# Optimization experiments

Hardware: AMD Instinct MI355X
Metric: run time of the kernel (lower is better)

The kernel has to match this reference:

```python
import jax, jax.numpy as jnp
import numpy as np


def _conv1x1(x, W, b):
    # 1x1 conv == per-pixel channel matmul: x [B,C,H,W], W [O,C], b [O]
    return jnp.einsum('bchw,oc->bohw', x, W) + b[None, :, None, None]


def setup_inputs() -> dict:
    key = jax.random.key(0)
    ks = jax.random.split(key, 9)
    B, C, H, W = 16, 512, 32, 32
    s = 1.0 / np.sqrt(C)
    inp = {
        'x': jax.random.normal(ks[0], (B, C, H, W), dtype=jnp.float32),
        'Wq': jax.random.normal(ks[1], (C, C), dtype=jnp.float32) * s,
        'bq': jax.random.normal(ks[2], (C,), dtype=jnp.float32) * 0.01,
        'Wk': jax.random.normal(ks[3], (C, C), dtype=jnp.float32) * s,
        'bk': jax.random.normal(ks[4], (C,), dtype=jnp.float32) * 0.01,
        'Wv': jax.random.normal(ks[5], (C, C), dtype=jnp.float32) * s,
        'bv': jax.random.normal(ks[6], (C,), dtype=jnp.float32) * 0.01,
        'Wo': jax.random.normal(ks[7], (C, C), dtype=jnp.float32) * s,
        'bo': jax.random.normal(ks[8], (C,), dtype=jnp.float32) * 0.01,
    }
    return inp


def reference(x, Wq, bq, Wk, bk, Wv, bv, Wo, bo):
    B, C, H, W = x.shape
    q = _conv1x1(x, Wq, bq)
    k = _conv1x1(x, Wk, bk)
    v = _conv1x1(x, Wv, bv)
    hw = H * W
    qf = q.reshape(B, C, hw)  # [B,C,HW]
    kf = k.reshape(B, C, hw)
    vf = v.reshape(B, C, hw)
    # scores[b,i,j] = sum_c q[b,c,i] * k[b,c,j], scaled by c^-0.5
    scores = jnp.einsum('bci,bcj->bij', qf, kf) * (C ** -0.5)
    attn = jax.nn.softmax(scores, axis=2)  # softmax over keys j
    # out[b,c,i] = sum_j v[b,c,j] * attn[b,i,j]
    out = jnp.einsum('bcj,bij->bci', vf, attn).reshape(B, C, H, W)
    out = _conv1x1(out, Wo, bo)
    return x + out
```

## Files before the change

kernel.cpp:

```cpp
#include <hip/hip_runtime.h>
#include <hip/hip_bf16.h>
#include <math.h>


typedef __bf16 bf16x8 __attribute__((ext_vector_type(8)));
typedef float  f32x4  __attribute__((ext_vector_type(4)));

__device__ __forceinline__ unsigned short f2bf(float f) {
    unsigned u = __float_as_uint(f);
    u += 0x7fff + ((u >> 16) & 1);
    return (unsigned short)(u >> 16);
}

__device__ __forceinline__ float bf2f(unsigned short h) {
    return __uint_as_float(((unsigned)h) << 16);
}

__device__ __forceinline__ void gload_lds16(const void* g, void* l) {
    __builtin_amdgcn_global_load_lds(
        (const __attribute__((address_space(1))) void*)g,
        (__attribute__((address_space(3))) void*)l, 16, 0, 0);
}

template<bool OUT_F32, int BIAS_MODE, int RESID, int EXPM>
__global__ __launch_bounds__(256) void gemm_bt_mfma(
    const unsigned short* __restrict__ A, const unsigned short* __restrict__ B,
    void* __restrict__ Cout, const float* __restrict__ bias,
    const unsigned short* __restrict__ resid, float* __restrict__ lsum,
    int M, int N, int K, int ldA, int ldB,
    long sA, long sB, long sC, long sR,
    int ln_nn, int ln_pb)
{
    __shared__ unsigned short Als[2][128 * 32];
    __shared__ unsigned short Bls[2][128 * 32];

    const int L   = blockIdx.x;
    const int xcd = L & 7;
    const int idx = L >> 3;
    const int bz  = xcd * 2 + (idx >> ln_pb);
    const int w   = idx & ((1 << ln_pb) - 1);
    const int m0  = (w >> ln_nn) << 7;
    const int n0  = (w & ((1 << ln_nn) - 1)) << 7;

    A += bz * sA;
    B += bz * sB;

    const int tid  = threadIdx.x;
    const int lane = tid & 63;
    const int wave = tid >> 6;
    const int wm   = wave >> 1;
    const int wn   = wave & 1;

    const int ar = lane >> 2;
    const int ak = (lane & 3) * 8;

    const unsigned short* agp = A + (long)(m0 + wave * 16 + ar) * ldA + ak;
    const unsigned short* bgp = B + (long)(n0 + wave * 16 + ar) * ldB + ak;
    const long aj = 64L * ldA;
    const long bj = 64L * ldB;
    unsigned short* al0  = Als[0] + wave * 512;
    unsigned short* al0h = Als[0] + (wave + 4) * 512;
    unsigned short* al1  = Als[1] + wave * 512;
    unsigned short* al1h = Als[1] + (wave + 4) * 512;
    unsigned short* bl0  = Bls[0] + wave * 512;
    unsigned short* bl0h = Bls[0] + (wave + 4) * 512;
    unsigned short* bl1  = Bls[1] + wave * 512;
    unsigned short* bl1h = Bls[1] + (wave + 4) * 512;

    const int fr = lane & 15;
    const int fq = lane >> 4;

    f32x4 acc[4][4] = {};

    for (int k0 = 0; k0 < K; k0 += 64) {
        gload_lds16(agp,           al0);
        gload_lds16(agp + aj,      al0h);
        gload_lds16(agp + 32,      al1);
        gload_lds16(agp + 32 + aj, al1h);
        gload_lds16(bgp,           bl0);
        gload_lds16(bgp + bj,      bl0h);
        gload_lds16(bgp + 32,      bl1);
        gload_lds16(bgp + 32 + bj, bl1h);
        agp += 64; bgp += 64;
        __syncthreads();

        #pragma unroll
        for (int p = 0; p < 2; ++p) {
            bf16x8 af[4], bfr[4];
            #pragma unroll
            for (int mt = 0; mt < 4; ++mt)
                af[mt] = *(const bf16x8*)&Als[p][(wm * 64 + mt * 16 + fr) * 32 + fq * 8];
            #pragma unroll
            for (int nt = 0; nt < 4; ++nt)
                bfr[nt] = *(const bf16x8*)&Bls[p][(wn * 64 + nt * 16 + fr) * 32 + fq * 8];

            #pragma unroll
            for (int mt = 0; mt < 4; ++mt)
                #pragma unroll
                for (int nt = 0; nt < 4; ++nt)
                    acc[mt][nt] = __builtin_amdgcn_mfma_f32_16x16x32_bf16(
                        af[mt], bfr[nt], acc[mt][nt], 0, 0, 0);
        }
        __syncthreads();
    }

    float* Cf = (float*)Cout + bz * sC;
    unsigned short* Ch = (unsigned short*)Cout + bz * sC;
    if (RESID) resid += bz * sR;

    if (EXPM == 1) {
        float* lrow = lsum + bz * (long)M;
        #pragma unroll
        for (int mt = 0; mt < 4; ++mt) {
            const int row = m0 + wm * 64 + mt * 16 + fq * 4;
            #pragma unroll
            for (int r = 0; r < 4; ++r) {
                float rs = 0.0f;
                #pragma unroll
                for (int nt = 0; nt < 4; ++nt) {
                    const int col = n0 + wn * 64 + nt * 16 + fr;
                    const float e = __expf(acc[mt][nt][r]);
                    rs += e;
                    Ch[(long)(row + r) * N + col] = f2bf(e);
                }
                rs += __shfl_xor(rs, 1);
                rs += __shfl_xor(rs, 2);
                rs += __shfl_xor(rs, 4);
                rs += __shfl_xor(rs, 8);
                if (fr == 0) atomicAdd(&lrow[row + r], rs);
            }
        }
    } else {
        float linv[4][4];
        if (EXPM == 2) {
            const float* lrow = lsum + bz * (long)M;
            #pragma unroll
            for (int mt = 0; mt < 4; ++mt)
                #pragma unroll
                for (int r = 0; r < 4; ++r)
                    linv[mt][r] = 1.0f / lrow[m0 + wm * 64 + mt * 16 + fq * 4 + r];
        }
        #pragma unroll
        for (int nt = 0; nt < 4; ++nt) {
            const int col = n0 + wn * 64 + nt * 16 + fr;
            const float bn = (BIAS_MODE == 2) ? bias[col] : 0.0f;
            #pragma unroll
            for (int mt = 0; mt < 4; ++mt) {
                const int row = m0 + wm * 64 + mt * 16 + fq * 4;
                #pragma unroll
                for (int r = 0; r < 4; ++r) {
                    float val = acc[mt][nt][r] + bn;
                    if (BIAS_MODE == 1) val += bias[row + r];
                    if (EXPM == 2) val *= linv[mt][r];
                    const long idx = (long)(row + r) * N + col;
                    if (RESID == 2) val += bf2f(resid[idx]);
                    if (OUT_F32) Cf[idx] = val;
                    else         Ch[idx] = f2bf(val);
                }
            }
        }
    }
}

__global__ __launch_bounds__(256) void prep_all(
    const float* __restrict__ x,
    unsigned short* __restrict__ xT, unsigned short* __restrict__ xbf,
    const float* __restrict__ Wq, const float* __restrict__ Wk,
    const float* __restrict__ Wv, const float* __restrict__ Wo,
    const float* __restrict__ bq, const float* __restrict__ bk,
    const float* __restrict__ bv, const float* __restrict__ bo,
    unsigned short* __restrict__ Wqb, unsigned short* __restrict__ Wkb,
    unsigned short* __restrict__ Wvob,
    float* __restrict__ biasqk, float* __restrict__ bvo,
    float* __restrict__ lsum)
{
    const float s = 0.044194173824159216f;
    const int b = blockIdx.x;
    const int t = threadIdx.x;

    if (b < 256) {
        __shared__ float Ao[32][33];
        __shared__ float Bv[32][33];
        const int m0 = (b >> 4) * 32;
        const int n0 = (b & 15) * 32;
        const int tx = t & 31;
        const int ty = t >> 5;
        float acc[4] = {0.f, 0.f, 0.f, 0.f};
        for (int k0 = 0; k0 < 512; k0 += 32) {
            #pragma unroll
            for (int i = 0; i < 4; ++i)
                Ao[ty + 8 * i][tx] = Wo[(long)(m0 + ty + 8 * i) * 512 + k0 + tx];
            #pragma unroll
            for (int i = 0; i < 4; ++i)
                Bv[ty + 8 * i][tx] = Wv[(long)(k0 + ty + 8 * i) * 512 + n0 + tx];
            __syncthreads();
            #pragma unroll
            for (int kk = 0; kk < 32; ++kk) {
                const float bvv = Bv[kk][tx];
                #pragma unroll
                for (int i = 0; i < 4; ++i)
                    acc[i] += Ao[ty * 4 + i][kk] * bvv;
            }
            __syncthreads();
        }
        #pragma unroll
        for (int i = 0; i < 4; ++i)
            Wvob[(long)(m0 + ty * 4 + i) * 512 + n0 + tx] = f2bf(acc[i]);
    } else if (b < 264) {
        const int o = (b - 256) * 64 + (t >> 2);
        const int q = t & 3;
        const float4* wrow = (const float4*)(Wo + (long)o * 512 + q * 128);
        const float4* bvv4 = (const float4*)(bv + q * 128);
        float p = 0.f;
        #pragma unroll
        for (int i = 0; i < 32; ++i) {
            const float4 w = wrow[i];
            const float4 v = bvv4[i];
            p += w.x * v.x + w.y * v.y + w.z * v.z + w.w * v.w;
        }
        __shared__ float red[256];
        red[t] = p;
        __syncthreads();
        if (q == 0) bvo[o] = red[t] + red[t + 1] + red[t + 2] + red[t + 3] + bo[o];
    } else if (b == 264) {
        biasqk[t]       = bq[t] * s;
        biasqk[256 + t] = bq[256 + t] * s;
        biasqk[512 + t] = bk[t];
        biasqk[768 + t] = bk[256 + t];
        #pragma unroll
        for (int i = 0; i < 64; ++i) lsum[i * 256 + t] = 0.0f;
    } else if (b < 777) {
        const bool isq = b < 521;
        const float* src = isq ? Wq : Wk;
        unsigned short* dst = isq ? Wqb : Wkb;
        const float m = isq ? s : 1.0f;
        const int i = (((b - 265) & 255) * 256 + t) * 4;
        const float4 f = *(const float4*)(src + i);
        ushort4 h;
        h.x = f2bf(f.x * m); h.y = f2bf(f.y * m);
        h.z = f2bf(f.z * m); h.w = f2bf(f.w * m);
        *(ushort4*)(dst + i) = h;
    } else {
        __shared__ float tl[32][33];
        const int xb = b - 777;
        const int batch = xb >> 9;
        const int rem = xb & 511;
        const int p0 = (rem & 31) * 32;
        const int c0 = (rem >> 5) * 32;
        const float* xp = x + (long)batch * 524288;
        unsigned short* xTb  = xT  + (long)batch * 524288;
        unsigned short* xbfb = xbf + (long)batch * 524288;
        const int tx = t & 31;
        const int ty = t >> 5;
        #pragma unroll
        for (int i = 0; i < 4; ++i) {
            const float v = xp[(long)(c0 + ty + 8 * i) * 1024 + p0 + tx];
            xbfb[(long)(c0 + ty + 8 * i) * 1024 + p0 + tx] = f2bf(v);
            tl[ty + 8 * i][tx] = v;
        }
        __syncthreads();
        #pragma unroll
        for (int i = 0; i < 4; ++i)
            xTb[(long)(p0 + ty + 8 * i) * 512 + c0 + tx] = f2bf(tl[tx][ty + 8 * i]);
    }
}

extern "C" void kernel_launch(void* const* d_in, const int* in_sizes, int n_in,
                              void* d_out, int out_size, void* d_ws, size_t ws_size,
                              hipStream_t stream)
{
    const float* x  = (const float*)d_in[0];
    const float* Wq = (const float*)d_in[1];
    const float* bq = (const float*)d_in[2];
    const float* Wk = (const float*)d_in[3];
    const float* bk = (const float*)d_in[4];
    const float* Wv = (const float*)d_in[5];
    const float* bv = (const float*)d_in[6];
    const float* Wo = (const float*)d_in[7];
    const float* bo = (const float*)d_in[8];
    float* out = (float*)d_out;

    const int Bn = 16, C = 512, HW = 1024;
    const long CHW = (long)C * HW;
    const long SHW = (long)HW * HW;

    unsigned short* xT   = (unsigned short*)d_ws;
    unsigned short* qkT  = xT + Bn * CHW;
    unsigned short* xbf  = qkT + Bn * SHW;
    unsigned short* expS = xbf + Bn * CHW;
    unsigned short* Wqb  = expS + Bn * SHW;
    unsigned short* Wkb  = Wqb + 262144;
    unsigned short* Wvob = Wkb + 262144;
    float* biasqk = (float*)(Wvob + 262144);
    float* bvo    = biasqk + 1024;
    float* lsum   = bvo + 512;
    unsigned short* UT = xT;

    const dim3 blk(256);

    prep_all<<<dim3(8969), blk, 0, stream>>>(
        x, xT, xbf, Wq, Wk, Wv, Wo, bq, bk, bv, bo,
        Wqb, Wkb, Wvob, biasqk, bvo, lsum);

    gemm_bt_mfma<false, 2, 0, 0><<<dim3(1024), blk, 0, stream>>>(
        xT, Wqb, qkT, biasqk, nullptr, nullptr,
        HW, 2 * C, C, C, C, CHW, 0, SHW, 0, 3, 6);

    gemm_bt_mfma<false, 0, 0, 1><<<dim3(1024), blk, 0, stream>>>(
        qkT, qkT + C, expS, nullptr, nullptr, lsum,
        HW, HW, C, 2 * C, 2 * C, SHW, SHW, SHW, 0, 3, 6);

    gemm_bt_mfma<false, 0, 0, 2><<<dim3(512), blk, 0, stream>>>(
        expS, xbf, UT, nullptr, nullptr, lsum,
        HW, C, HW, HW, HW, SHW, CHW, CHW, 0, 2, 5);

    gemm_bt_mfma<true, 1, 2, 0><<<dim3(512), blk, 0, stream>>>(
        Wvob, UT, out, bvo, xbf, nullptr,
        C, HW, C, C, C, 0, CHW, CHW, CHW, 3, 5);
}
```

Before: 222.9 us.

## Reassociate output projection before attention and merge projection GEMMs into one launch

```diff
diff --git a/kernel.cpp b/kernel.cpp
--- a/kernel.cpp
+++ b/kernel.cpp
@@ -22,29 +22,22 @@
         (__attribute__((address_space(3))) void*)l, 16, 0, 0);
 }
 
-template<bool OUT_F32, int BIAS_MODE, int RESID, int EXPM>
-__global__ __launch_bounds__(256) void gemm_bt_mfma(
-    const unsigned short* __restrict__ A, const unsigned short* __restrict__ B,
-    void* __restrict__ Cout, const float* __restrict__ bias,
-    const unsigned short* __restrict__ resid, float* __restrict__ lsum,
-    int M, int N, int K, int ldA, int ldB,
-    long sA, long sB, long sC, long sR,
-    int ln_nn, int ln_pb)
-{
-    __shared__ unsigned short Als[2][128 * 32];
-    __shared__ unsigned short Bls[2][128 * 32];
-
-    const int L   = blockIdx.x;
+__device__ __forceinline__ void decode_tile(int L, int ln_nn, int ln_pb,
+                                            int& bz, int& m0, int& n0) {
     const int xcd = L & 7;
     const int idx = L >> 3;
-    const int bz  = xcd * 2 + (idx >> ln_pb);
-    const int w   = idx & ((1 << ln_pb) - 1);
-    const int m0  = (w >> ln_nn) << 7;
-    const int n0  = (w & ((1 << ln_nn) - 1)) << 7;
-
-    A += bz * sA;
-    B += bz * sB;
-
+    bz = xcd * 2 + (idx >> ln_pb);
+    const int w = idx & ((1 << ln_pb) - 1);
+    m0 = (w >> ln_nn) << 7;
+    n0 = (w & ((1 << ln_nn) - 1)) << 7;
+}
+
+__device__ __forceinline__ void mfma_kloop(
+    const unsigned short* __restrict__ A, const unsigned short* __restrict__ B,
+    int K, int ldA, int ldB, int m0, int n0,
+    unsigned short* als, unsigned short* bls,
+    f32x4 (&acc)[4][4])
+{
     const int tid  = threadIdx.x;
     const int lane = tid & 63;
     const int wave = tid >> 6;
@@ -58,19 +51,17 @@
     const unsigned short* bgp = B + (long)(n0 + wave * 16 + ar) * ldB + ak;
     const long aj = 64L * ldA;
     const long bj = 64L * ldB;
-    unsigned short* al0  = Als[0] + wave * 512;
-    unsigned short* al0h = Als[0] + (wave + 4) * 512;
-    unsigned short* al1  = Als[1] + wave * 512;
-    unsigned short* al1h = Als[1] + (wave + 4) * 512;
-    unsigned short* bl0  = Bls[0] + wave * 512;
-    unsigned short* bl0h = Bls[0] + (wave + 4) * 512;
-    unsigned short* bl1  = Bls[1] + wave * 512;
-    unsigned short* bl1h = Bls[1] + (wave + 4) * 512;
+    unsigned short* al0  = als + wave * 512;
+    unsigned short* al0h = als + (wave + 4) * 512;
+    unsigned short* al1  = als + 4096 + wave * 512;
+    unsigned short* al1h = als + 4096 + (wave + 4) * 512;
+    unsigned short* bl0  = bls + wave * 512;
+    unsigned short* bl0h = bls + (wave + 4) * 512;
+    unsigned short* bl1  = bls + 4096 + wave * 512;
+    unsigned short* bl1h = bls + 4096 + (wave + 4) * 512;
 
     const int fr = lane & 15;
     const int fq = lane >> 4;
-
-    f32x4 acc[4][4] = {};
 
     for (int k0 = 0; k0 < K; k0 += 64) {
         gload_lds16(agp,           al0);
@@ -89,10 +80,10 @@
             bf16x8 af[4], bfr[4];
             #pragma unroll
             for (int mt = 0; mt < 4; ++mt)
-                af[mt] = *(const bf16x8*)&Als[p][(wm * 64 + mt * 16 + fr) * 32 + fq * 8];
+                af[mt] = *(const bf16x8*)&als[p * 4096 + (wm * 64 + mt * 16 + fr) * 32 + fq * 8];
             #pragma unroll
             for (int nt = 0; nt < 4; ++nt)
-                bfr[nt] = *(const bf16x8*)&Bls[p][(wn * 64 + nt * 16 + fr) * 32 + fq * 8];
+                bfr[nt] = *(const bf16x8*)&bls[p * 4096 + (wn * 64 + nt * 16 + fr) * 32 + fq * 8];
 
             #pragma unroll
             for (int mt = 0; mt < 4; ++mt)
@@ -103,60 +94,143 @@
         }
         __syncthreads();
     }
-
-    float* Cf = (float*)Cout + bz * sC;
-    unsigned short* Ch = (unsigned short*)Cout + bz * sC;
-    if (RESID) resid += bz * sR;
-
-    if (EXPM == 1) {
-        float* lrow = lsum + bz * (long)M;
+}
+
+__global__ __launch_bounds__(256) void gemm_plain2(
+    const unsigned short* __restrict__ A0, const unsigned short* __restrict__ B0,
+    unsigned short* __restrict__ C0, const float* __restrict__ bias0,
+    int N0, int K0, int ldA0, int ldB0, long sA0, long sB0, long sC0,
+    int ln_nn0, int ln_pb0, int nb0,
+    const unsigned short* __restrict__ A1, const unsigned short* __restrict__ B1,
+    unsigned short* __restrict__ C1, const float* __restrict__ bias1,
+    int N1, int K1, int ldA1, int ldB1, long sA1, long sB1, long sC1,
+    int ln_nn1, int ln_pb1)
+{
+    __shared__ unsigned short Als[2 * 128 * 32];
+    __shared__ unsigned short Bls[2 * 128 * 32];
+
+    int L = blockIdx.x;
+    const unsigned short *A, *B;
+    unsigned short* C;
+    const float* bias;
+    int N, K, ldA, ldB, ln_nn, ln_pb;
+    long sA, sB, sC;
+    if (L < nb0) {
+        A = A0; B = B0; C = C0; bias = bias0;
+        N = N0; K = K0; ldA = ldA0; ldB = ldB0;
+        sA = sA0; sB = sB0; sC = sC0; ln_nn = ln_nn0; ln_pb = ln_pb0;
+    } else {
+        L -= nb0;
+        A = A1; B = B1; C = C1; bias = bias1;
+        N = N1; K = K1; ldA = ldA1; ldB = ldB1;
+        sA = sA1; sB = sB1; sC = sC1; ln_nn = ln_nn1; ln_pb = ln_pb1;
+    }
+
+    int bz, m0, n0;
+    decode_tile(L, ln_nn, ln_pb, bz, m0, n0);
+
+    f32x4 acc[4][4] = {};
+    mfma_kloop(A + bz * sA, B + bz * sB, K, ldA, ldB, m0, n0, Als, Bls, acc);
+
+    const int lane = threadIdx.x & 63;
+    const int wave = threadIdx.x >> 6;
+    const int wm = wave >> 1, wn = wave & 1;
+    const int fr = lane & 15, fq = lane >> 4;
+
+    unsigned short* Ch = C + bz * sC;
+    #pragma unroll
+    for (int nt = 0; nt < 4; ++nt) {
+        const int col = n0 + wn * 64 + nt * 16 + fr;
+        const float bn = bias ? bias[col] : 0.0f;
         #pragma unroll
         for (int mt = 0; mt < 4; ++mt) {
             const int row = m0 + wm * 64 + mt * 16 + fq * 4;
             #pragma unroll
+            for (int r = 0; r < 4; ++r)
+                Ch[(long)(row + r) * N + col] = f2bf(acc[mt][nt][r] + bn);
+        }
+    }
+}
+
+__global__ __launch_bounds__(256) void gemm_exp(
+    const unsigned short* __restrict__ A, const unsigned short* __restrict__ B,
+    unsigned short* __restrict__ Cout, float* __restrict__ lsum,
+    int N, int K, int ldA, int ldB, long sA, long sB, long sC, long sL,
+    int ln_nn, int ln_pb)
+{
+    __shared__ unsigned short Als[2 * 128 * 32];
+    __shared__ unsigned short Bls[2 * 128 * 32];
+
+    int bz, m0, n0;
+    decode_tile(blockIdx.x, ln_nn, ln_pb, bz, m0, n0);
+
+    f32x4 acc[4][4] = {};
+    mfma_kloop(A + bz * sA, B + bz * sB, K, ldA, ldB, m0, n0, Als, Bls, acc);
+
+    const int lane = threadIdx.x & 63;
+    const int wave = threadIdx.x >> 6;
+    const int wm = wave >> 1, wn = wave & 1;
+    const int fr = lane & 15, fq = lane >> 4;
+
+    unsigned short* Ch = Cout + bz * sC;
+    float* lrow = lsum + bz * sL;
+    #pragma unroll
+    for (int mt = 0; mt < 4; ++mt) {
+        const int row = m0 + wm * 64 + mt * 16 + fq * 4;
+        #pragma unroll
+        for (int r = 0; r < 4; ++r) {
+            float rs = 0.0f;
+            #pragma unroll
+            for (int nt = 0; nt < 4; ++nt) {
+                const int col = n0 + wn * 64 + nt * 16 + fr;
+                const float e = __expf(acc[mt][nt][r]);
+                rs += e;
+                Ch[(long)(row + r) * N + col] = f2bf(e);
+            }
+            rs += __shfl_xor(rs, 1);
+            rs += __shfl_xor(rs, 2);
+            rs += __shfl_xor(rs, 4);
+            rs += __shfl_xor(rs, 8);
+            if (fr == 0) atomicAdd(&lrow[row + r], rs);
+        }
+    }
+}
+
+__global__ __launch_bounds__(256) void gemm_final(
+    const unsigned short* __restrict__ A, const unsigned short* __restrict__ B,
+    float* __restrict__ Cout, const float* __restrict__ biasM,
+    const unsigned short* __restrict__ resid, const float* __restrict__ lsum,
+    int N, int K, int ldA, int ldB, long sA, long sB, long sC, long sR, long sL,
+    int ln_nn, int ln_pb)
+{
+    __shared__ unsigned short Als[2 * 128 * 32];
+    __shared__ unsigned short Bls[2 * 128 * 32];
+
+    int bz, m0, n0;
+    decode_tile(blockIdx.x, ln_nn, ln_pb, bz, m0, n0);
+
+    f32x4 acc[4][4] = {};
+    mfma_kloop(A + bz * sA, B + bz * sB, K, ldA, ldB, m0, n0, Als, Bls, acc);
+
+    const int lane = threadIdx.x & 63;
+    const int wave = threadIdx.x >> 6;
+    const int wm = wave >> 1, wn = wave & 1;
+    const int fr = lane & 15, fq = lane >> 4;
+
+    float* Cf = Cout + bz * sC;
+    const unsigned short* rz = resid + bz * sR;
+    const float* lrow = lsum + bz * sL;
+    #pragma unroll
+    for (int nt = 0; nt < 4; ++nt) {
+        const int col = n0 + wn * 64 + nt * 16 + fr;
+        const float linv = 1.0f / lrow[col];
+        #pragma unroll
+        for (int mt = 0; mt < 4; ++mt) {
+            const int row = m0 + wm * 64 + mt * 16 + fq * 4;
+            #pragma unroll
             for (int r = 0; r < 4; ++r) {
-                float rs = 0.0f;
-                #pragma unroll
-                for (int nt = 0; nt < 4; ++nt) {
-                    const int col = n0 + wn * 64 + nt * 16 + fr;
-                    const float e = __expf(acc[mt][nt][r]);
-                    rs += e;
-                    Ch[(long)(row + r) * N + col] = f2bf(e);
-                }
-                rs += __shfl_xor(rs, 1);
-                rs += __shfl_xor(rs, 2);
-                rs += __shfl_xor(rs, 4);
-                rs += __shfl_xor(rs, 8);
-                if (fr == 0) atomicAdd(&lrow[row + r], rs);
-            }
-        }
-    } else {
-        float linv[4][4];
-        if (EXPM == 2) {
-            const float* lrow = lsum + bz * (long)M;
-            #pragma unroll
-            for (int mt = 0; mt < 4; ++mt)
-                #pragma unroll
-                for (int r = 0; r < 4; ++r)
-                    linv[mt][r] = 1.0f / lrow[m0 + wm * 64 + mt * 16 + fq * 4 + r];
-        }
-        #pragma unroll
-        for (int nt = 0; nt < 4; ++nt) {
-            const int col = n0 + wn * 64 + nt * 16 + fr;
-            const float bn = (BIAS_MODE == 2) ? bias[col] : 0.0f;
-            #pragma unroll
-            for (int mt = 0; mt < 4; ++mt) {
-                const int row = m0 + wm * 64 + mt * 16 + fq * 4;
-                #pragma unroll
-                for (int r = 0; r < 4; ++r) {
-                    float val = acc[mt][nt][r] + bn;
-                    if (BIAS_MODE == 1) val += bias[row + r];
-                    if (EXPM == 2) val *= linv[mt][r];
-                    const long idx = (long)(row + r) * N + col;
-                    if (RESID == 2) val += bf2f(resid[idx]);
-                    if (OUT_F32) Cf[idx] = val;
-                    else         Ch[idx] = f2bf(val);
-                }
+                const long idx = (long)(row + r) * N + col;
+                Cf[idx] = acc[mt][nt][r] * linv + biasM[row + r] + bf2f(rz[idx]);
             }
         }
     }
@@ -288,13 +362,13 @@
     unsigned short* qkT  = xT + Bn * CHW;
     unsigned short* xbf  = qkT + Bn * SHW;
     unsigned short* expS = xbf + Bn * CHW;
-    unsigned short* Wqb  = expS + Bn * SHW;
+    unsigned short* Yb   = expS + Bn * SHW;
+    unsigned short* Wqb  = Yb + Bn * CHW;
     unsigned short* Wkb  = Wqb + 262144;
     unsigned short* Wvob = Wkb + 262144;
     float* biasqk = (float*)(Wvob + 262144);
     float* bvo    = biasqk + 1024;
     float* lsum   = bvo + 512;
-    unsigned short* UT = xT;
 
     const dim3 blk(256);
 
@@ -302,19 +376,15 @@
         x, xT, xbf, Wq, Wk, Wv, Wo, bq, bk, bv, bo,
         Wqb, Wkb, Wvob, biasqk, bvo, lsum);
 
-    gemm_bt_mfma<false, 2, 0, 0><<<dim3(1024), blk, 0, stream>>>(
-        xT, Wqb, qkT, biasqk, nullptr, nullptr,
-        HW, 2 * C, C, C, C, CHW, 0, SHW, 0, 3, 6);
-
-    gemm_bt_mfma<false, 0, 0, 1><<<dim3(1024), blk, 0, stream>>>(
-        qkT, qkT + C, expS, nullptr, nullptr, lsum,
-        HW, HW, C, 2 * C, 2 * C, SHW, SHW, SHW, 0, 3, 6);
-
-    gemm_bt_mfma<false, 0, 0, 2><<<dim3(512), blk, 0, stream>>>(
-        expS, xbf, UT, nullptr, nullptr, lsum,
-        HW, C, HW, HW, HW, SHW, CHW, CHW, 0, 2, 5);
-
-    gemm_bt_mfma<true, 1, 2, 0><<<dim3(512), blk, 0, stream>>>(
-        Wvob, UT, out, bvo, xbf, nullptr,
-        C, HW, C, C, C, 0, CHW, CHW, CHW, 3, 5);
-}
+    gemm_plain2<<<dim3(1536), blk, 0, stream>>>(
+        xT, Wqb, qkT, biasqk, 2 * C, C, C, C, CHW, 0, SHW, 3, 6, 1024,
+        Wvob, xT, Yb, nullptr, HW, C, C, C, 0, CHW, CHW, 3, 5);
+
+    gemm_exp<<<dim3(1024), blk, 0, stream>>>(
+        qkT, qkT + C, expS, lsum,
+        HW, C, 2 * C, 2 * C, SHW, SHW, SHW, HW, 3, 6);
+
+    gemm_final<<<dim3(512), blk, 0, stream>>>(
+        Yb, expS, out, bvo, xbf, lsum,
+        HW, HW, HW, HW, CHW, SHW, CHW, CHW, HW, 3, 5);
+}
```

Measured after the change: 220.4 us. Within noise of the previous version (-1.1%).
